# Kernel tuning notes

Hardware: AMD Instinct MI355X
Metric: run time of the kernel (lower is better)

The kernel has to match this reference:

```python
import jax, jax.numpy as jnp
import numpy as np

B, S, H = 1, 2048, 2048
NH, NKV, HD = 32, 8, 64
GROUPS = NH // NKV
KV_DIM = NKV * HD
COMP = int(S * 0.5)
FF = 5632  # round_up(2048*4*2/3, 256), fla GatedMLP convention
DEPTH = 2
EPS = 1e-6


def rmsnorm(x, w):
    var = jnp.mean(jnp.square(x), axis=-1, keepdims=True)
    return x * jax.lax.rsqrt(var + EPS) * w


def setup_inputs() -> dict:
    key = jax.random.key(0)
    ks = jax.random.split(key, 10)
    sc = 0.02
    return {
        "hidden_states": jax.random.normal(ks[0], (B, S, H), jnp.float32),
        "comp_w": jax.random.normal(ks[1], (COMP, S), jnp.float32) * sc,
        "comp_b": jnp.zeros((COMP,), jnp.float32),
        "q_w": jax.random.normal(ks[2], (H, H), jnp.float32) * sc,
        "k_w": jax.random.normal(ks[3], (KV_DIM, H), jnp.float32) * sc,
        "v_w": jax.random.normal(ks[4], (KV_DIM, H), jnp.float32) * sc,
        "o_w": jax.random.normal(ks[5], (H, H), jnp.float32) * sc,
        "attn_norm_w": jnp.ones((H,), jnp.float32),
        "mlp_norm_w": jnp.ones((H,), jnp.float32),
        "gate_w": jax.random.normal(ks[6], (FF, H), jnp.float32) * sc,
        "up_w": jax.random.normal(ks[7], (FF, H), jnp.float32) * sc,
        "down_w": jax.random.normal(ks[8], (H, FF), jnp.float32) * sc,
    }


def reference(hidden_states, comp_w, comp_b, q_w, k_w, v_w, o_w,
              attn_norm_w, mlp_norm_w, gate_w, up_w, down_w):
    # init_compressed_tokens: Linear over the sequence axis
    # (b,s,h) -> transpose -> (b,h,s) @ W^T -> (b,h,c) -> transpose -> (b,c,h)
    compressed = jnp.einsum('bsh,cs->bch', hidden_states, comp_w) + comp_b[None, :, None]

    for _ in range(DEPTH):
        residual = jnp.concatenate([hidden_states, compressed], axis=1)  # (b, s+c, h)
        ct = rmsnorm(compressed, attn_norm_w)
        q = (ct @ q_w.T).reshape(B, COMP, NH, HD)
        k = (residual @ k_w.T).reshape(B, S + COMP, NKV, HD)
        v = (residual @ v_w.T).reshape(B, S + COMP, NKV, HD)
        # GQA expand (repeat_interleave along head dim)
        k = jnp.repeat(k, GROUPS, axis=2)
        v = jnp.repeat(v, GROUPS, axis=2)
        scores = jnp.einsum('bsnk,btnk->bsnt', q, k) / (HD ** 0.5)
        attn = jax.nn.softmax(scores, axis=-1)
        o = jnp.einsum('bsnt,btnk->bsnk', attn, v).reshape(B, COMP, H)
        compressed = o @ o_w.T + ct
        ct2 = rmsnorm(compressed, mlp_norm_w)
        mlp_out = (jax.nn.silu(ct2 @ gate_w.T) * (ct2 @ up_w.T)) @ down_w.T
        compressed = mlp_out + ct2
    return compressed
```

## Files before the change

kernel.cpp:

```cpp
#include <hip/hip_runtime.h>
#include <math.h>

constexpr int S_   = 2048;
constexpr int H_   = 2048;
constexpr int NH_  = 32;
constexpr int NKV_ = 8;
constexpr int HD_  = 64;
constexpr int GROUPS_ = NH_ / NKV_;
constexpr int KV_  = NKV_ * HD_;
constexpr int KV2_ = 2 * KV_;
constexpr int COMP_ = 1024;
constexpr int FF_  = 5632;
constexpr int GU2_ = 2 * FF_;
constexpr int TOT_ = S_ + COMP_;
constexpr float EPS_ = 1e-6f;
constexpr int SK_ = 4;

typedef __attribute__((ext_vector_type(4))) float f32x4;
typedef __attribute__((ext_vector_type(8))) short bf16x8;
typedef __attribute__((ext_vector_type(8))) ushort u16x8;

__device__ __forceinline__ ushort f2bf(float x) {
    union { float f; unsigned u; } v; v.f = x;
    unsigned r = v.u + 0x7fffu + ((v.u >> 16) & 1u);
    return (ushort)(r >> 16);
}
__device__ __forceinline__ float bf2f(ushort x) {
    union { unsigned u; float f; } v; v.u = ((unsigned)x) << 16;
    return v.f;
}

__global__ __launch_bounds__(256) void f2b_k(
    const float* __restrict__ x, ushort* __restrict__ y, int n4)
{
    int i = blockIdx.x * 256 + threadIdx.x;
    const int stride = gridDim.x * 256;
    for (; i < n4; i += stride) {
        float4 v = ((const float4*)x)[i];
        ushort4 r = {f2bf(v.x), f2bf(v.y), f2bf(v.z), f2bf(v.w)};
        ((ushort4*)y)[i] = r;
    }
}

__global__ __launch_bounds__(256) void tpose64(
    const ushort* __restrict__ in, ushort* __restrict__ out,
    int R, int C, int ldi)
{
    __shared__ ushort T[64][72];
    const int r0 = blockIdx.x * 64, c0 = blockIdx.y * 64;
    const int row = threadIdx.x >> 2, seg = threadIdx.x & 3;

    const ushort* g = &in[(size_t)(r0 + row) * ldi + c0 + seg * 16];
    *(u16x8*)&T[row][seg * 16]     = *(const u16x8*)g;
    *(u16x8*)&T[row][seg * 16 + 8] = *(const u16x8*)(g + 8);
    __syncthreads();

    ushort tmp[16];
#pragma unroll
    for (int j = 0; j < 16; j++) tmp[j] = T[seg * 16 + j][row];
    ushort* go = &out[(size_t)(c0 + row) * R + r0 + seg * 16];
    *(u16x8*)go       = *(const u16x8*)&tmp[0];
    *(u16x8*)(go + 8) = *(const u16x8*)&tmp[8];
}

__global__ __launch_bounds__(256) void mfma_gemm(
    const ushort* __restrict__ A, const ushort* __restrict__ B,
    const float* __restrict__ addp, const float* __restrict__ bias,
    float oscale, float* __restrict__ outf, ushort* __restrict__ outb,
    int M, int N, int K)
{
    __shared__ ushort Alds[128 * 32];
    __shared__ ushort Blds[128 * 32];

    const int tid  = threadIdx.x;
    const int w    = tid >> 6;
    const int lane = tid & 63;
    const int bm = blockIdx.y, bn = blockIdx.x;
    const int wr = w >> 1, wc = w & 1;
    const int fr = lane & 15;
    const int fq = lane >> 4;
    const int srow = lane >> 2;
    const int skof = (lane & 3) * 8;

    f32x4 acc[4][4];
#pragma unroll
    for (int i = 0; i < 4; i++)
#pragma unroll
        for (int j = 0; j < 4; j++)
            acc[i][j] = (f32x4){0.f, 0.f, 0.f, 0.f};

    for (int k0 = 0; k0 < K; k0 += 32) {
        __syncthreads();
#pragma unroll
        for (int i = 0; i < 2; i++) {
            const int slot = w * 2 + i;
            const ushort* ga = &A[(size_t)(bm * 128 + slot * 16 + srow) * K + k0 + skof];
            __builtin_amdgcn_global_load_lds(
                (const __attribute__((address_space(1))) void*)ga,
                (__attribute__((address_space(3))) void*)&Alds[slot * 512], 16, 0, 0);
            const ushort* gb = &B[(size_t)(bn * 128 + slot * 16 + srow) * K + k0 + skof];
            __builtin_amdgcn_global_load_lds(
                (const __attribute__((address_space(1))) void*)gb,
                (__attribute__((address_space(3))) void*)&Blds[slot * 512], 16, 0, 0);
        }
        __syncthreads();

        bf16x8 a[4], b[4];
#pragma unroll
        for (int mt = 0; mt < 4; mt++)
            a[mt] = *(const bf16x8*)&Alds[(wr * 64 + mt * 16 + fr) * 32 + fq * 8];
#pragma unroll
        for (int nt = 0; nt < 4; nt++)
            b[nt] = *(const bf16x8*)&Blds[(wc * 64 + nt * 16 + fr) * 32 + fq * 8];

#pragma unroll
        for (int mt = 0; mt < 4; mt++)
#pragma unroll
            for (int nt = 0; nt < 4; nt++)
                acc[mt][nt] = __builtin_amdgcn_mfma_f32_16x16x32_bf16(
                    a[mt], b[nt], acc[mt][nt], 0, 0, 0);
    }

#pragma unroll
    for (int mt = 0; mt < 4; mt++) {
#pragma unroll
        for (int nt = 0; nt < 4; nt++) {
#pragma unroll
            for (int r = 0; r < 4; r++) {
                const int row = bm * 128 + wr * 64 + mt * 16 + fq * 4 + r;
                const int col = bn * 128 + wc * 64 + nt * 16 + fr;
                float v = acc[mt][nt][r] * oscale;
                if (bias) v += bias[row];
                if (addp) v += addp[(size_t)row * N + col];
                if (outf) outf[(size_t)row * N + col] = v;
                if (outb) outb[(size_t)row * N + col] = f2bf(v);
            }
        }
    }
}

__global__ __launch_bounds__(256) void mfma_gemm_sk(
    const ushort* __restrict__ A, const ushort* __restrict__ B,
    float* __restrict__ part, int M, int N, int K, int Kc)
{
    __shared__ ushort Alds[128 * 32];
    __shared__ ushort Blds[128 * 32];

    const int tid  = threadIdx.x;
    const int w    = tid >> 6;
    const int lane = tid & 63;
    const int bm = blockIdx.y, bn = blockIdx.x, z = blockIdx.z;
    const int wr = w >> 1, wc = w & 1;
    const int fr = lane & 15;
    const int fq = lane >> 4;
    const int srow = lane >> 2;
    const int skof = (lane & 3) * 8;

    f32x4 acc[4][4];
#pragma unroll
    for (int i = 0; i < 4; i++)
#pragma unroll
        for (int j = 0; j < 4; j++)
            acc[i][j] = (f32x4){0.f, 0.f, 0.f, 0.f};

    const int kbeg = z * Kc;
    for (int k0 = kbeg; k0 < kbeg + Kc; k0 += 32) {
        __syncthreads();
#pragma unroll
        for (int i = 0; i < 2; i++) {
            const int slot = w * 2 + i;
            const ushort* ga = &A[(size_t)(bm * 128 + slot * 16 + srow) * K + k0 + skof];
            __builtin_amdgcn_global_load_lds(
                (const __attribute__((address_space(1))) void*)ga,
                (__attribute__((address_space(3))) void*)&Alds[slot * 512], 16, 0, 0);
            const ushort* gb = &B[(size_t)(bn * 128 + slot * 16 + srow) * K + k0 + skof];
            __builtin_amdgcn_global_load_lds(
                (const __attribute__((address_space(1))) void*)gb,
                (__attribute__((address_space(3))) void*)&Blds[slot * 512], 16, 0, 0);
        }
        __syncthreads();

        bf16x8 a[4], b[4];
#pragma unroll
        for (int mt = 0; mt < 4; mt++)
            a[mt] = *(const bf16x8*)&Alds[(wr * 64 + mt * 16 + fr) * 32 + fq * 8];
#pragma unroll
        for (int nt = 0; nt < 4; nt++)
            b[nt] = *(const bf16x8*)&Blds[(wc * 64 + nt * 16 + fr) * 32 + fq * 8];

#pragma unroll
        for (int mt = 0; mt < 4; mt++)
#pragma unroll
            for (int nt = 0; nt < 4; nt++)
                acc[mt][nt] = __builtin_amdgcn_mfma_f32_16x16x32_bf16(
                    a[mt], b[nt], acc[mt][nt], 0, 0, 0);
    }

    float* pz = part + (size_t)z * M * N;
#pragma unroll
    for (int mt = 0; mt < 4; mt++)
#pragma unroll
        for (int nt = 0; nt < 4; nt++)
#pragma unroll
            for (int r = 0; r < 4; r++) {
                const int row = bm * 128 + wr * 64 + mt * 16 + fq * 4 + r;
                const int col = bn * 128 + wc * 64 + nt * 16 + fr;
                pz[(size_t)row * N + col] = acc[mt][nt][r];
            }
}

__global__ __launch_bounds__(256) void sk_reduce(
    const float* __restrict__ part, int mn4, int n4,
    const float* __restrict__ bias, const float* __restrict__ addp,
    float oscale, float* __restrict__ outf, ushort* __restrict__ outb)
{
    const size_t mn = (size_t)mn4 * 4;
    int i = blockIdx.x * 256 + threadIdx.x;
    const int stride = gridDim.x * 256;
    for (; i < mn4; i += stride) {
        float4 v = ((const float4*)part)[i];
#pragma unroll
        for (int z = 1; z < SK_; z++) {
            const float4 pz = ((const float4*)(part + z * mn))[i];
            v.x += pz.x; v.y += pz.y; v.z += pz.z; v.w += pz.w;
        }
        v.x *= oscale; v.y *= oscale; v.z *= oscale; v.w *= oscale;
        if (bias) {
            const float bb = bias[i / n4];
            v.x += bb; v.y += bb; v.z += bb; v.w += bb;
        }
        if (addp) {
            const float4 ad = ((const float4*)addp)[i];
            v.x += ad.x; v.y += ad.y; v.z += ad.z; v.w += ad.w;
        }
        if (outf) ((float4*)outf)[i] = v;
        if (outb) {
            ushort4 r = {f2bf(v.x), f2bf(v.y), f2bf(v.z), f2bf(v.w)};
            ((ushort4*)outb)[i] = r;
        }
    }
}

__global__ __launch_bounds__(256) void attn_mfma(
    const ushort* __restrict__ q, const ushort* __restrict__ k, int ldk,
    const ushort* __restrict__ vt, ushort* __restrict__ o)
{
    constexpr int LDT = 72;
    __shared__ ushort Qs[64 * LDT];
    __shared__ ushort Ks[64 * LDT];
    __shared__ ushort Vs[64 * LDT];
    __shared__ ushort Ps[64 * LDT];

    const int qt = blockIdx.x, h = blockIdx.y;
    const int kvh = h / GROUPS_;
    const int tid = threadIdx.x;
    const int w = tid >> 6, lane = tid & 63;
    const int fr = lane & 15, fq = lane >> 4;
    const int q0 = qt * 64;

    {
        const int row = tid >> 2, seg = tid & 3;
        const ushort* g = &q[(size_t)(q0 + row) * H_ + h * HD_ + seg * 16];
        *(u16x8*)&Qs[row * LDT + seg * 16]     = *(const u16x8*)g;
        *(u16x8*)&Qs[row * LDT + seg * 16 + 8] = *(const u16x8*)(g + 8);
    }

    float m[4] = {-1e30f, -1e30f, -1e30f, -1e30f};
    float l[4] = {0.f, 0.f, 0.f, 0.f};
    f32x4 acc[4];
#pragma unroll
    for (int nt = 0; nt < 4; nt++) acc[nt] = (f32x4){0.f, 0.f, 0.f, 0.f};

    for (int t0 = 0; t0 < TOT_; t0 += 64) {
        __syncthreads();
        {
            const int row = tid >> 2, seg = tid & 3;
            const ushort* gk = &k[(size_t)(t0 + row) * ldk + kvh * HD_ + seg * 16];
            u16x8 k0v = *(const u16x8*)gk;
            u16x8 k1v = *(const u16x8*)(gk + 8);
            const ushort* gv = &vt[(size_t)(kvh * HD_ + row) * TOT_ + t0 + seg * 16];
            u16x8 v0v = *(const u16x8*)gv;
            u16x8 v1v = *(const u16x8*)(gv + 8);
            *(u16x8*)&Ks[row * LDT + seg * 16]     = k0v;
            *(u16x8*)&Ks[row * LDT + seg * 16 + 8] = k1v;
            *(u16x8*)&Vs[row * LDT + seg * 16]     = v0v;
            *(u16x8*)&Vs[row * LDT + seg * 16 + 8] = v1v;
        }
        __syncthreads();

        bf16x8 aq0 = *(const bf16x8*)&Qs[(w * 16 + fr) * LDT + fq * 8];
        bf16x8 aq1 = *(const bf16x8*)&Qs[(w * 16 + fr) * LDT + 32 + fq * 8];
        f32x4 sc[4];
#pragma unroll
        for (int nt = 0; nt < 4; nt++) {
            bf16x8 b0 = *(const bf16x8*)&Ks[(nt * 16 + fr) * LDT + fq * 8];
            bf16x8 b1 = *(const bf16x8*)&Ks[(nt * 16 + fr) * LDT + 32 + fq * 8];
            f32x4 t = (f32x4){0.f, 0.f, 0.f, 0.f};
            t = __builtin_amdgcn_mfma_f32_16x16x32_bf16(aq0, b0, t, 0, 0, 0);
            t = __builtin_amdgcn_mfma_f32_16x16x32_bf16(aq1, b1, t, 0, 0, 0);
            sc[nt] = t;
        }

        float alpha[4];
#pragma unroll
        for (int r = 0; r < 4; r++) {
            float mt = fmaxf(fmaxf(sc[0][r], sc[1][r]), fmaxf(sc[2][r], sc[3][r]));
#pragma unroll
            for (int msk = 1; msk < 16; msk <<= 1)
                mt = fmaxf(mt, __shfl_xor(mt, msk, 16));
            const float mn = fmaxf(m[r], mt);
            alpha[r] = __expf(m[r] - mn);
            m[r] = mn;
            float ss = 0.f;
#pragma unroll
            for (int nt = 0; nt < 4; nt++) {
                const float p = __expf(sc[nt][r] - mn);
                sc[nt][r] = p;
                ss += p;
            }
#pragma unroll
            for (int msk = 1; msk < 16; msk <<= 1)
                ss += __shfl_xor(ss, msk, 16);
            l[r] = l[r] * alpha[r] + ss;
        }

#pragma unroll
        for (int nt = 0; nt < 4; nt++)
#pragma unroll
            for (int r = 0; r < 4; r++)
                Ps[(w * 16 + fq * 4 + r) * LDT + nt * 16 + fr] = f2bf(sc[nt][r]);

        bf16x8 ap0 = *(const bf16x8*)&Ps[(w * 16 + fr) * LDT + fq * 8];
        bf16x8 ap1 = *(const bf16x8*)&Ps[(w * 16 + fr) * LDT + 32 + fq * 8];
#pragma unroll
        for (int nt = 0; nt < 4; nt++) {
            bf16x8 b0 = *(const bf16x8*)&Vs[(nt * 16 + fr) * LDT + fq * 8];
            bf16x8 b1 = *(const bf16x8*)&Vs[(nt * 16 + fr) * LDT + 32 + fq * 8];
            f32x4 t = acc[nt];
            t[0] *= alpha[0]; t[1] *= alpha[1]; t[2] *= alpha[2]; t[3] *= alpha[3];
            t = __builtin_amdgcn_mfma_f32_16x16x32_bf16(ap0, b0, t, 0, 0, 0);
            t = __builtin_amdgcn_mfma_f32_16x16x32_bf16(ap1, b1, t, 0, 0, 0);
            acc[nt] = t;
        }
    }

#pragma unroll
    for (int r = 0; r < 4; r++) {
        const float inv = 1.0f / l[r];
#pragma unroll
        for (int nt = 0; nt < 4; nt++)
            o[(size_t)(q0 + w * 16 + fq * 4 + r) * H_ + h * HD_ + nt * 16 + fr] =
                f2bf(acc[nt][r] * inv);
    }
}

__global__ __launch_bounds__(256) void rmsnorm_dual_k(
    const float* __restrict__ x, const float* __restrict__ w,
    float* __restrict__ y, ushort* __restrict__ yb)
{
    const int row = blockIdx.x;
    const float* xr = x + (size_t)row * H_;
    __shared__ float red[256];

    float s = 0.f;
#pragma unroll
    for (int i = 0; i < 8; i++) {
        const float v = xr[threadIdx.x + i * 256];
        s += v * v;
    }
    red[threadIdx.x] = s;
    __syncthreads();
    for (int t = 128; t > 0; t >>= 1) {
        if (threadIdx.x < t) red[threadIdx.x] += red[threadIdx.x + t];
        __syncthreads();
    }
    const float scale = rsqrtf(red[0] * (1.0f / H_) + EPS_);
#pragma unroll
    for (int i = 0; i < 8; i++) {
        const int idx = threadIdx.x + i * 256;
        const float v = xr[idx] * scale * w[idx];
        y[(size_t)row * H_ + idx] = v;
        yb[(size_t)row * H_ + idx] = f2bf(v);
    }
}

__global__ __launch_bounds__(256) void silu_mul_gu(
    const ushort* __restrict__ gu, ushort* __restrict__ g, int n4)
{
    constexpr int FF4 = FF_ / 4;
    int i = blockIdx.x * 256 + threadIdx.x;
    const int stride = gridDim.x * 256;
    for (; i < n4; i += stride) {
        const int row = i / FF4;
        const int c = (i - row * FF4) * 4;
        ushort4 gv = *(const ushort4*)&gu[(size_t)row * GU2_ + c];
        ushort4 uv = *(const ushort4*)&gu[(size_t)row * GU2_ + FF_ + c];
        float x0 = bf2f(gv.x), x1 = bf2f(gv.y), x2 = bf2f(gv.z), x3 = bf2f(gv.w);
        x0 = x0 / (1.f + __expf(-x0)) * bf2f(uv.x);
        x1 = x1 / (1.f + __expf(-x1)) * bf2f(uv.y);
        x2 = x2 / (1.f + __expf(-x2)) * bf2f(uv.z);
        x3 = x3 / (1.f + __expf(-x3)) * bf2f(uv.w);
        ushort4 r = {f2bf(x0), f2bf(x1), f2bf(x2), f2bf(x3)};
        ((ushort4*)g)[i] = r;
    }
}

extern "C" void kernel_launch(void* const* d_in, const int* in_sizes, int n_in,
                              void* d_out, int out_size, void* d_ws, size_t ws_size,
                              hipStream_t stream)
{
    (void)in_sizes; (void)n_in; (void)out_size; (void)ws_size;

    const float* hidden      = (const float*)d_in[0];
    const float* comp_w      = (const float*)d_in[1];
    const float* comp_b      = (const float*)d_in[2];
    const float* q_w         = (const float*)d_in[3];
    const float* k_w         = (const float*)d_in[4];
    const float* v_w         = (const float*)d_in[5];
    const float* o_w         = (const float*)d_in[6];
    const float* attn_norm_w = (const float*)d_in[7];
    const float* mlp_norm_w  = (const float*)d_in[8];
    const float* gate_w      = (const float*)d_in[9];
    const float* up_w        = (const float*)d_in[10];
    const float* down_w      = (const float*)d_in[11];
    float* out = (float*)d_out;

    char* p = (char*)d_ws;
    auto alloc = [&](size_t bytes) -> char* {
        char* r = p; p += (bytes + 255) & ~(size_t)255; return r;
    };
    ushort* qw_bf    = (ushort*)alloc((size_t)H_ * H_ * 2);
    ushort* kvw_bf   = (ushort*)alloc((size_t)KV2_ * H_ * 2);
    ushort* ow_bf    = (ushort*)alloc((size_t)H_ * H_ * 2);
    ushort* guw_bf   = (ushort*)alloc((size_t)GU2_ * H_ * 2);
    ushort* down_bf  = (ushort*)alloc((size_t)H_ * FF_ * 2);
    ushort* compw_bf = (ushort*)alloc((size_t)COMP_ * S_ * 2);
    ushort* hidcomp  = (ushort*)alloc((size_t)TOT_ * H_ * 2);
    ushort* hidT     = (ushort*)alloc((size_t)H_ * S_ * 2);
    ushort* ct_bf    = (ushort*)alloc((size_t)COMP_ * H_ * 2);
    ushort* ct2_bf   = (ushort*)alloc((size_t)COMP_ * H_ * 2);
    ushort* ob_bf    = (ushort*)alloc((size_t)COMP_ * H_ * 2);
    ushort* qb_bf    = (ushort*)alloc((size_t)COMP_ * H_ * 2);
    ushort* kvb_bf   = (ushort*)alloc((size_t)TOT_ * KV2_ * 2);
    ushort* vt_bf    = (ushort*)alloc((size_t)KV_ * TOT_ * 2);
    ushort* gb_bf    = (ushort*)alloc((size_t)COMP_ * FF_ * 2);
    float* comp0 = (float*)alloc((size_t)COMP_ * H_ * 4);
    float* comp1 = (float*)alloc((size_t)COMP_ * H_ * 4);
    float* ct    = (float*)alloc((size_t)COMP_ * H_ * 4);
    float* ct2   = (float*)alloc((size_t)COMP_ * H_ * 4);
    float*  skbuf = (float*)alloc((size_t)SK_ * TOT_ * KV2_ * 4);
    ushort* gub   = (ushort*)skbuf;

    ushort* cur_bf = hidcomp + (size_t)S_ * H_;

    const dim3 blk(256);

    f2b_k<<<512, blk, 0, stream>>>(q_w,    qw_bf,            H_ * H_ / 4);
    f2b_k<<<512, blk, 0, stream>>>(k_w,    kvw_bf,           KV_ * H_ / 4);
    f2b_k<<<512, blk, 0, stream>>>(v_w,    kvw_bf + (size_t)KV_ * H_, KV_ * H_ / 4);
    f2b_k<<<512, blk, 0, stream>>>(o_w,    ow_bf,            H_ * H_ / 4);
    f2b_k<<<512, blk, 0, stream>>>(gate_w, guw_bf,           FF_ * H_ / 4);
    f2b_k<<<512, blk, 0, stream>>>(up_w,   guw_bf + (size_t)FF_ * H_, FF_ * H_ / 4);
    f2b_k<<<512, blk, 0, stream>>>(down_w, down_bf,          H_ * FF_ / 4);
    f2b_k<<<512, blk, 0, stream>>>(comp_w, compw_bf,         COMP_ * S_ / 4);
    f2b_k<<<512, blk, 0, stream>>>(hidden, hidcomp,          S_ * H_ / 4);
    tpose64<<<dim3(S_ / 64, H_ / 64), blk, 0, stream>>>(hidcomp, hidT, S_, H_, H_);

    mfma_gemm_sk<<<dim3(H_ / 128, COMP_ / 128, SK_), blk, 0, stream>>>(
        compw_bf, hidT, skbuf, COMP_, H_, S_, S_ / SK_);
    sk_reduce<<<1024, blk, 0, stream>>>(
        skbuf, COMP_ * H_ / 4, H_ / 4, comp_b, nullptr, 1.f, comp0, cur_bf);

    float* cur = comp0;
    for (int d = 0; d < 2; d++) {
        rmsnorm_dual_k<<<COMP_, blk, 0, stream>>>(cur, attn_norm_w, ct, ct_bf);

        mfma_gemm_sk<<<dim3(H_ / 128, COMP_ / 128, SK_), blk, 0, stream>>>(
            ct_bf, qw_bf, skbuf, COMP_, H_, H_, H_ / SK_);
        sk_reduce<<<1024, blk, 0, stream>>>(
            skbuf, COMP_ * H_ / 4, H_ / 4, nullptr, nullptr, 0.125f, nullptr, qb_bf);

        mfma_gemm_sk<<<dim3(KV2_ / 128, TOT_ / 128, SK_), blk, 0, stream>>>(
            hidcomp, kvw_bf, skbuf, TOT_, KV2_, H_, H_ / SK_);
        sk_reduce<<<1024, blk, 0, stream>>>(
            skbuf, TOT_ * KV2_ / 4, KV2_ / 4, nullptr, nullptr, 1.f, nullptr, kvb_bf);

        tpose64<<<dim3(TOT_ / 64, KV_ / 64), blk, 0, stream>>>(
            kvb_bf + KV_, vt_bf, TOT_, KV_, KV2_);

        attn_mfma<<<dim3(COMP_ / 64, NH_), blk, 0, stream>>>(
            qb_bf, kvb_bf, KV2_, vt_bf, ob_bf);

        mfma_gemm_sk<<<dim3(H_ / 128, COMP_ / 128, SK_), blk, 0, stream>>>(
            ob_bf, ow_bf, skbuf, COMP_, H_, H_, H_ / SK_);
        sk_reduce<<<1024, blk, 0, stream>>>(
            skbuf, COMP_ * H_ / 4, H_ / 4, nullptr, ct, 1.f, comp1, nullptr);

        rmsnorm_dual_k<<<COMP_, blk, 0, stream>>>(comp1, mlp_norm_w, ct2, ct2_bf);

        mfma_gemm<<<dim3(GU2_ / 128, COMP_ / 128), blk, 0, stream>>>(
            ct2_bf, guw_bf, nullptr, nullptr, 1.f, nullptr, gub, COMP_, GU2_, H_);

        silu_mul_gu<<<1024, blk, 0, stream>>>(gub, gb_bf, COMP_ * FF_ / 4);

        float* dst = (d == 1) ? out : comp0;
        ushort* dst_bf = (d == 1) ? nullptr : cur_bf;
        mfma_gemm_sk<<<dim3(H_ / 128, COMP_ / 128, SK_), blk, 0, stream>>>(
            gb_bf, down_bf, skbuf, COMP_, H_, FF_, FF_ / SK_);
        sk_reduce<<<1024, blk, 0, stream>>>(
            skbuf, COMP_ * H_ / 4, H_ / 4, nullptr, ct2, 1.f, dst, dst_bf);
        cur = dst;
    }
}
```

Baseline: 995.2 us.

## Split attention along KV axis into two partitions and merge partial softmax results

The attention kernel now runs over half of the key/value sequence per block, with grid z of 2, writing unnormalized fp32 partial outputs plus per-row max and sum. A new merge kernel rescales and combines the two partials and emits bf16 output. The change also folds log2(e) into the Q scaling so exp2f can replace __expf, and hoists the Q fragment loads out of the loop. It doubles the attention grid from 512 to 1024 blocks for better occupancy, at the cost of extra fp32 partial traffic and one more launch.

```diff
diff --git a/kernel.cpp b/kernel.cpp
--- a/kernel.cpp
+++ b/kernel.cpp
@@ -15,6 +15,8 @@
 constexpr int TOT_ = S_ + COMP_;
 constexpr float EPS_ = 1e-6f;
 constexpr int SK_ = 4;
+constexpr int SP_ = 2;
+constexpr float LOG2E_ = 1.44269504088896340736f;
 
 typedef __attribute__((ext_vector_type(4))) float f32x4;
 typedef __attribute__((ext_vector_type(8))) short bf16x8;
@@ -243,15 +245,17 @@
 
 __global__ __launch_bounds__(256) void attn_mfma(
     const ushort* __restrict__ q, const ushort* __restrict__ k, int ldk,
-    const ushort* __restrict__ vt, ushort* __restrict__ o)
+    const ushort* __restrict__ vt, float* __restrict__ attp,
+    float* __restrict__ ml)
 {
     constexpr int LDT = 72;
+    constexpr int KSPAN = TOT_ / SP_;
     __shared__ ushort Qs[64 * LDT];
     __shared__ ushort Ks[64 * LDT];
     __shared__ ushort Vs[64 * LDT];
     __shared__ ushort Ps[64 * LDT];
 
-    const int qt = blockIdx.x, h = blockIdx.y;
+    const int qt = blockIdx.x, h = blockIdx.y, z = blockIdx.z;
     const int kvh = h / GROUPS_;
     const int tid = threadIdx.x;
     const int w = tid >> 6, lane = tid & 63;
@@ -264,6 +268,9 @@
         *(u16x8*)&Qs[row * LDT + seg * 16]     = *(const u16x8*)g;
         *(u16x8*)&Qs[row * LDT + seg * 16 + 8] = *(const u16x8*)(g + 8);
     }
+    __syncthreads();
+    const bf16x8 aq0 = *(const bf16x8*)&Qs[(w * 16 + fr) * LDT + fq * 8];
+    const bf16x8 aq1 = *(const bf16x8*)&Qs[(w * 16 + fr) * LDT + 32 + fq * 8];
 
     float m[4] = {-1e30f, -1e30f, -1e30f, -1e30f};
     float l[4] = {0.f, 0.f, 0.f, 0.f};
@@ -271,7 +278,8 @@
 #pragma unroll
     for (int nt = 0; nt < 4; nt++) acc[nt] = (f32x4){0.f, 0.f, 0.f, 0.f};
 
-    for (int t0 = 0; t0 < TOT_; t0 += 64) {
+    const int t_beg = z * KSPAN;
+    for (int t0 = t_beg; t0 < t_beg + KSPAN; t0 += 64) {
         __syncthreads();
         {
             const int row = tid >> 2, seg = tid & 3;
@@ -288,8 +296,6 @@
         }
         __syncthreads();
 
-        bf16x8 aq0 = *(const bf16x8*)&Qs[(w * 16 + fr) * LDT + fq * 8];
-        bf16x8 aq1 = *(const bf16x8*)&Qs[(w * 16 + fr) * LDT + 32 + fq * 8];
         f32x4 sc[4];
 #pragma unroll
         for (int nt = 0; nt < 4; nt++) {
@@ -309,12 +315,12 @@
             for (int msk = 1; msk < 16; msk <<= 1)
                 mt = fmaxf(mt, __shfl_xor(mt, msk, 16));
             const float mn = fmaxf(m[r], mt);
-            alpha[r] = __expf(m[r] - mn);
+            alpha[r] = exp2f(m[r] - mn);
             m[r] = mn;
             float ss = 0.f;
 #pragma unroll
             for (int nt = 0; nt < 4; nt++) {
-                const float p = __expf(sc[nt][r] - mn);
+                const float p = exp2f(sc[nt][r] - mn);
                 sc[nt][r] = p;
                 ss += p;
             }
@@ -344,13 +350,43 @@
         }
     }
 
+    float* pz = attp + (size_t)z * COMP_ * H_;
 #pragma unroll
     for (int r = 0; r < 4; r++) {
-        const float inv = 1.0f / l[r];
+        const int row = q0 + w * 16 + fq * 4 + r;
 #pragma unroll
         for (int nt = 0; nt < 4; nt++)
-            o[(size_t)(q0 + w * 16 + fq * 4 + r) * H_ + h * HD_ + nt * 16 + fr] =
-                f2bf(acc[nt][r] * inv);
+            pz[(size_t)row * H_ + h * HD_ + nt * 16 + fr] = acc[nt][r];
+        if (fr == 0)
+            ((float2*)ml)[((size_t)z * NH_ + h) * COMP_ + row] =
+                make_float2(m[r], l[r]);
+    }
+}
+
+__global__ __launch_bounds__(256) void attn_merge(
+    const float* __restrict__ attp, const float* __restrict__ ml,
+    ushort* __restrict__ o, int n4)
+{
+    constexpr int H4 = H_ / 4;
+    constexpr size_t PS = (size_t)COMP_ * H_;
+    int i = blockIdx.x * 256 + threadIdx.x;
+    const int stride = gridDim.x * 256;
+    for (; i < n4; i += stride) {
+        const int row = i / H4;
+        const int col = (i - row * H4) * 4;
+        const int h = col >> 6;
+        const float2 ml0 = ((const float2*)ml)[((size_t)0 * NH_ + h) * COMP_ + row];
+        const float2 ml1 = ((const float2*)ml)[((size_t)1 * NH_ + h) * COMP_ + row];
+        const float M = fmaxf(ml0.x, ml1.x);
+        const float a0 = exp2f(ml0.x - M), a1 = exp2f(ml1.x - M);
+        const float inv = 1.0f / (a0 * ml0.y + a1 * ml1.y);
+        const float4 p0 = ((const float4*)attp)[i];
+        const float4 p1 = ((const float4*)(attp + PS))[i];
+        ushort4 r = {f2bf((a0 * p0.x + a1 * p1.x) * inv),
+                     f2bf((a0 * p0.y + a1 * p1.y) * inv),
+                     f2bf((a0 * p0.z + a1 * p1.z) * inv),
+                     f2bf((a0 * p0.w + a1 * p1.w) * inv)};
+        ((ushort4*)o)[i] = r;
     }
 }
 
@@ -450,6 +486,8 @@
     float* ct2   = (float*)alloc((size_t)COMP_ * H_ * 4);
     float*  skbuf = (float*)alloc((size_t)SK_ * TOT_ * KV2_ * 4);
     ushort* gub   = (ushort*)skbuf;
+    float*  attp  = skbuf;
+    float*  mlbuf = skbuf + (size_t)SP_ * COMP_ * H_;
 
     ushort* cur_bf = hidcomp + (size_t)S_ * H_;
 
@@ -478,7 +516,8 @@
         mfma_gemm_sk<<<dim3(H_ / 128, COMP_ / 128, SK_), blk, 0, stream>>>(
             ct_bf, qw_bf, skbuf, COMP_, H_, H_, H_ / SK_);
         sk_reduce<<<1024, blk, 0, stream>>>(
-            skbuf, COMP_ * H_ / 4, H_ / 4, nullptr, nullptr, 0.125f, nullptr, qb_bf);
+            skbuf, COMP_ * H_ / 4, H_ / 4, nullptr, nullptr, 0.125f * LOG2E_,
+            nullptr, qb_bf);
 
         mfma_gemm_sk<<<dim3(KV2_ / 128, TOT_ / 128, SK_), blk, 0, stream>>>(
             hidcomp, kvw_bf, skbuf, TOT_, KV2_, H_, H_ / SK_);
@@ -488,8 +527,9 @@
         tpose64<<<dim3(TOT_ / 64, KV_ / 64), blk, 0, stream>>>(
             kvb_bf + KV_, vt_bf, TOT_, KV_, KV2_);
 
-        attn_mfma<<<dim3(COMP_ / 64, NH_), blk, 0, stream>>>(
-            qb_bf, kvb_bf, KV2_, vt_bf, ob_bf);
+        attn_mfma<<<dim3(COMP_ / 64, NH_, SP_), blk, 0, stream>>>(
+            qb_bf, kvb_bf, KV2_, vt_bf, attp, mlbuf);
+        attn_merge<<<512, blk, 0, stream>>>(attp, mlbuf, ob_bf, COMP_ * H_ / 4);
 
         mfma_gemm_sk<<<dim3(H_ / 128, COMP_ / 128, SK_), blk, 0, stream>>>(
             ob_bf, ow_bf, skbuf, COMP_, H_, H_, H_ / SK_);
```

Result: faster. 967.7 us (-2.8%).
